# Optimization experiments

Hardware: AMD Instinct MI355X
Metric: run time of the kernel (lower is better)

The kernel has to match this reference:

```python
import jax, jax.numpy as jnp
import numpy as np

N = 50000
E = 800000
NHID = 128
NOUT = 64
NLAYER = 4
BN_EPS = 1e-5


def setup_inputs() -> dict:
    key = jax.random.key(0)
    ks = jax.random.split(key, 4)
    x = jax.random.normal(ks[0], (N, NHID), dtype=jnp.float32)
    edge_index = jax.random.randint(ks[1], (2, E), 0, N, dtype=jnp.int32)
    Ws = jax.random.normal(ks[2], (NLAYER, NHID, NHID), dtype=jnp.float32) / np.sqrt(NHID)
    bs = jnp.zeros((NLAYER, NHID), dtype=jnp.float32)
    gammas = jnp.ones((NLAYER, NHID), dtype=jnp.float32)
    betas = jnp.zeros((NLAYER, NHID), dtype=jnp.float32)
    Wout = jax.random.normal(ks[3], (NHID, NOUT), dtype=jnp.float32) / np.sqrt(NHID)
    bout = jnp.zeros((NOUT,), dtype=jnp.float32)
    return {"x": x, "edge_index": edge_index, "Ws": Ws, "bs": bs,
            "gammas": gammas, "betas": betas, "Wout": Wout, "bout": bout}


def _gcn_conv(x, src, dst, norm, W, b):
    # GCNConv: h = x W, then symmetric-normalized scatter-add over edges (+ self loops already in src/dst)
    h = x @ W                                   # [N, nhid]
    msgs = h[src] * norm[:, None]               # [E+N, nhid] gather + scale
    agg = jax.ops.segment_sum(msgs, dst, num_segments=N)  # scatter-add
    return agg + b


def _batchnorm(x, gamma, beta):
    mean = jnp.mean(x, axis=0)
    var = jnp.mean(jnp.square(x - mean), axis=0)  # biased var (torch BN)
    return (x - mean) * jax.lax.rsqrt(var + BN_EPS) * gamma + beta


def reference(x, edge_index, Ws, bs, gammas, betas, Wout, bout):
    # add self loops
    loops = jnp.arange(N, dtype=edge_index.dtype)
    src = jnp.concatenate([edge_index[0], loops])
    dst = jnp.concatenate([edge_index[1], loops])
    # symmetric degree normalization: deg^-1/2[src] * deg^-1/2[dst]
    deg = jax.ops.segment_sum(jnp.ones_like(dst, dtype=x.dtype), dst, num_segments=N)
    dinv = jax.lax.rsqrt(jnp.maximum(deg, 1.0))
    norm = dinv[src] * dinv[dst]

    prev = x
    for l in range(NLAYER):
        h = _gcn_conv(x, src, dst, norm, Ws[l], bs[l])
        h = _batchnorm(h, gammas[l], betas[l])
        h = jax.nn.relu(h)
        # dropout p=0.0 -> identity
        x = h + prev  # residual
        prev = x
    return x @ Wout + bout
```

## Files before the change

### kernel.cpp

```cpp
#include <hip/hip_runtime.h>

#define NN 50000
#define NE 800000
#define NH 128
#define NO 64
#define NL 4
#define BN_EPS 1e-5f
#define NB1 ((NN + 255) / 256)
#define NGB (NN / 16)

typedef __attribute__((ext_vector_type(8))) short short8;
typedef __attribute__((ext_vector_type(4))) float f32x4;

__device__ inline unsigned short f2bf(float f) {
    unsigned int u = __float_as_uint(f);
    return (unsigned short)((u + 0x7fffu + ((u >> 16) & 1u)) >> 16);
}
__device__ inline float bflo(unsigned int u) { return __uint_as_float(u << 16); }
__device__ inline float bfhi(unsigned int u) { return __uint_as_float(u & 0xffff0000u); }
__device__ inline unsigned pk(float a, float b) {
    return (unsigned)f2bf(a) | ((unsigned)f2bf(b) << 16);
}

__global__ void k_degrank(const int* __restrict__ dst, int* __restrict__ deg,
                          int* __restrict__ rank) {
    int base = (blockIdx.x * 256 + threadIdx.x) * 2;
    if (base >= NE) return;
    int2 d2 = *(const int2*)&dst[base];
    int2 r2;
    r2.x = atomicAdd(&deg[d2.x], 1);
    r2.y = atomicAdd(&deg[d2.y], 1);
    *(int2*)&rank[base] = r2;
}

__global__ void k_scan1(const int* __restrict__ deg, int* __restrict__ off,
                        int* __restrict__ aux, float* __restrict__ dinv) {
    __shared__ int ls[256];
    int i = blockIdx.x * 256 + threadIdx.x;
    int v = (i < NN) ? deg[i] : 0;
    ls[threadIdx.x] = v;
    __syncthreads();
    for (int s = 1; s < 256; s <<= 1) {
        int t = (threadIdx.x >= s) ? ls[threadIdx.x - s] : 0;
        __syncthreads();
        ls[threadIdx.x] += t;
        __syncthreads();
    }
    if (i < NN) {
        off[i] = ls[threadIdx.x] - v;
        dinv[i] = rsqrtf((float)v + 1.0f);
    }
    if (threadIdx.x == 255) aux[blockIdx.x] = ls[255];
}

__global__ void k_scan2(int* __restrict__ aux) {
    __shared__ int ls[256];
    int v = (threadIdx.x < NB1) ? aux[threadIdx.x] : 0;
    ls[threadIdx.x] = v;
    __syncthreads();
    for (int s = 1; s < 256; s <<= 1) {
        int t = (threadIdx.x >= s) ? ls[threadIdx.x - s] : 0;
        __syncthreads();
        ls[threadIdx.x] += t;
        __syncthreads();
    }
    if (threadIdx.x < NB1) aux[threadIdx.x] = ls[threadIdx.x] - v;
}

__global__ void k_fill(const int* __restrict__ src, const int* __restrict__ dst,
                       const int* __restrict__ off, const int* __restrict__ aux,
                       const int* __restrict__ rank, int* __restrict__ csr) {
    int base = (blockIdx.x * 256 + threadIdx.x) * 4;
    if (base >= NE) return;
    int4 d4 = *(const int4*)&dst[base];
    int4 r4 = *(const int4*)&rank[base];
    int4 s4 = *(const int4*)&src[base];
    csr[off[d4.x] + aux[d4.x >> 8] + r4.x] = s4.x;
    csr[off[d4.y] + aux[d4.y >> 8] + r4.y] = s4.y;
    csr[off[d4.z] + aux[d4.z >> 8] + r4.z] = s4.z;
    csr[off[d4.w] + aux[d4.w >> 8] + r4.w] = s4.w;
}

__global__ void k_pack(const float* __restrict__ Ws, const float* __restrict__ Wout,
                       unsigned short* __restrict__ Wpk, unsigned short* __restrict__ Wopk) {
    int t = blockIdx.x * 256 + threadIdx.x;
    if (t < NL * 16384) {
        int l = t >> 14, r = t & 16383;
        int ks = r >> 12, ct = (r >> 9) & 7, lane = (r >> 3) & 63, i = r & 7;
        int k = ks * 32 + (lane >> 4) * 8 + i;
        int n = ct * 16 + (lane & 15);
        Wpk[t] = f2bf(Ws[l * 16384 + k * 128 + n]);
    } else if (t < NL * 16384 + 8192) {
        int r = t - NL * 16384;
        int ks = r >> 11, ct = (r >> 9) & 3, lane = (r >> 3) & 63, i = r & 7;
        int k = ks * 32 + (lane >> 4) * 8 + i;
        int n = ct * 16 + (lane & 15);
        Wopk[r] = f2bf(Wout[k * 64 + n]);
    }
}

__global__ __launch_bounds__(256) void k_fg0(const float* __restrict__ X,
                                             const unsigned short* __restrict__ Wpk,
                                             const float* __restrict__ dinv,
                                             unsigned short* __restrict__ Hd) {
    int w = threadIdx.x >> 6, l = threadIdx.x & 63;
    int row0 = blockIdx.x * 64 + w * 16;
    int lo = l & 15, hi = l >> 4;
    int arow = row0 + lo;
    int crow = (arow < NN) ? arow : NN - 1;
    short8 frag[4];
#pragma unroll
    for (int g = 0; g < 4; g++) {
        int cs = g * 32 + hi * 8;
        float4 p0 = *(const float4*)&X[(size_t)crow * NH + cs];
        float4 p1 = *(const float4*)&X[(size_t)crow * NH + cs + 4];
        short8 f;
        f[0] = (short)f2bf(p0.x); f[1] = (short)f2bf(p0.y);
        f[2] = (short)f2bf(p0.z); f[3] = (short)f2bf(p0.w);
        f[4] = (short)f2bf(p1.x); f[5] = (short)f2bf(p1.y);
        f[6] = (short)f2bf(p1.z); f[7] = (short)f2bf(p1.w);
        frag[g] = f;
    }
    const short8* Wv = (const short8*)Wpk;
    int srow = row0 + hi * 4;
    float dv[4];
#pragma unroll
    for (int r = 0; r < 4; r++) dv[r] = (srow + r < NN) ? dinv[srow + r] : 0.0f;
#pragma unroll
    for (int ct = 0; ct < 8; ct++) {
        f32x4 acc = {0.0f, 0.0f, 0.0f, 0.0f};
#pragma unroll
        for (int g = 0; g < 4; g++)
            acc = __builtin_amdgcn_mfma_f32_16x16x32_bf16(frag[g], Wv[(g * 8 + ct) * 64 + l], acc, 0, 0, 0);
        int col = ct * 16 + lo;
#pragma unroll
        for (int r = 0; r < 4; r++) {
            int grow = srow + r;
            if (grow < NN) Hd[grow * NH + col] = f2bf(acc[r] * dv[r]);
        }
    }
}

__global__ __launch_bounds__(256) void k_fg(const unsigned short* __restrict__ AGGb,
                                            const float* __restrict__ scale,
                                            const float* __restrict__ shift,
                                            const float* __restrict__ Xprev,
                                            float* __restrict__ Xout,
                                            const unsigned short* __restrict__ Wpk,
                                            const float* __restrict__ dinv,
                                            unsigned short* __restrict__ Hd) {
    int w = threadIdx.x >> 6, l = threadIdx.x & 63;
    int row0 = blockIdx.x * 64 + w * 16;
    int lo = l & 15, hi = l >> 4;
    int arow = row0 + lo;
    bool valid = arow < NN;
    int crow = valid ? arow : NN - 1;
    short8 frag[4];
#pragma unroll
    for (int g = 0; g < 4; g++) {
        int cs = g * 32 + hi * 8;
        uint4 ab = *(const uint4*)&AGGb[(size_t)crow * NH + cs];
        float4 p0 = *(const float4*)&Xprev[(size_t)crow * NH + cs];
        float4 p1 = *(const float4*)&Xprev[(size_t)crow * NH + cs + 4];
        float4 sc0 = *(const float4*)&scale[cs];
        float4 sc1 = *(const float4*)&scale[cs + 4];
        float4 sh0 = *(const float4*)&shift[cs];
        float4 sh1 = *(const float4*)&shift[cs + 4];
        float o0 = fmaxf(fmaf(bflo(ab.x), sc0.x, sh0.x), 0.0f) + p0.x;
        float o1 = fmaxf(fmaf(bfhi(ab.x), sc0.y, sh0.y), 0.0f) + p0.y;
        float o2 = fmaxf(fmaf(bflo(ab.y), sc0.z, sh0.z), 0.0f) + p0.z;
        float o3 = fmaxf(fmaf(bfhi(ab.y), sc0.w, sh0.w), 0.0f) + p0.w;
        float o4 = fmaxf(fmaf(bflo(ab.z), sc1.x, sh1.x), 0.0f) + p1.x;
        float o5 = fmaxf(fmaf(bfhi(ab.z), sc1.y, sh1.y), 0.0f) + p1.y;
        float o6 = fmaxf(fmaf(bflo(ab.w), sc1.z, sh1.z), 0.0f) + p1.z;
        float o7 = fmaxf(fmaf(bfhi(ab.w), sc1.w, sh1.w), 0.0f) + p1.w;
        if (valid) {
            float4 s0 = {o0, o1, o2, o3}, s1 = {o4, o5, o6, o7};
            *(float4*)&Xout[(size_t)arow * NH + cs] = s0;
            *(float4*)&Xout[(size_t)arow * NH + cs + 4] = s1;
        }
        short8 f;
        f[0] = (short)f2bf(o0); f[1] = (short)f2bf(o1);
        f[2] = (short)f2bf(o2); f[3] = (short)f2bf(o3);
        f[4] = (short)f2bf(o4); f[5] = (short)f2bf(o5);
        f[6] = (short)f2bf(o6); f[7] = (short)f2bf(o7);
        frag[g] = f;
    }
    const short8* Wv = (const short8*)Wpk;
    int srow = row0 + hi * 4;
    float dv[4];
#pragma unroll
    for (int r = 0; r < 4; r++) dv[r] = (srow + r < NN) ? dinv[srow + r] : 0.0f;
#pragma unroll
    for (int ct = 0; ct < 8; ct++) {
        f32x4 acc = {0.0f, 0.0f, 0.0f, 0.0f};
#pragma unroll
        for (int g = 0; g < 4; g++)
            acc = __builtin_amdgcn_mfma_f32_16x16x32_bf16(frag[g], Wv[(g * 8 + ct) * 64 + l], acc, 0, 0, 0);
        int col = ct * 16 + lo;
#pragma unroll
        for (int r = 0; r < 4; r++) {
            int grow = srow + r;
            if (grow < NN) Hd[grow * NH + col] = f2bf(acc[r] * dv[r]);
        }
    }
}

__global__ __launch_bounds__(256) void k_fgout(const unsigned short* __restrict__ AGGb,
                                               const float* __restrict__ scale,
                                               const float* __restrict__ shift,
                                               const float* __restrict__ Xprev,
                                               const unsigned short* __restrict__ Wpk,
                                               const float* __restrict__ b,
                                               float* __restrict__ out) {
    int w = threadIdx.x >> 6, l = threadIdx.x & 63;
    int row0 = blockIdx.x * 64 + w * 16;
    int lo = l & 15, hi = l >> 4;
    int arow = row0 + lo;
    int crow = (arow < NN) ? arow : NN - 1;
    short8 frag[4];
#pragma unroll
    for (int g = 0; g < 4; g++) {
        int cs = g * 32 + hi * 8;
        uint4 ab = *(const uint4*)&AGGb[(size_t)crow * NH + cs];
        float4 p0 = *(const float4*)&Xprev[(size_t)crow * NH + cs];
        float4 p1 = *(const float4*)&Xprev[(size_t)crow * NH + cs + 4];
        float4 sc0 = *(const float4*)&scale[cs];
        float4 sc1 = *(const float4*)&scale[cs + 4];
        float4 sh0 = *(const float4*)&shift[cs];
        float4 sh1 = *(const float4*)&shift[cs + 4];
        short8 f;
        f[0] = (short)f2bf(fmaxf(fmaf(bflo(ab.x), sc0.x, sh0.x), 0.0f) + p0.x);
        f[1] = (short)f2bf(fmaxf(fmaf(bfhi(ab.x), sc0.y, sh0.y), 0.0f) + p0.y);
        f[2] = (short)f2bf(fmaxf(fmaf(bflo(ab.y), sc0.z, sh0.z), 0.0f) + p0.z);
        f[3] = (short)f2bf(fmaxf(fmaf(bfhi(ab.y), sc0.w, sh0.w), 0.0f) + p0.w);
        f[4] = (short)f2bf(fmaxf(fmaf(bflo(ab.z), sc1.x, sh1.x), 0.0f) + p1.x);
        f[5] = (short)f2bf(fmaxf(fmaf(bfhi(ab.z), sc1.y, sh1.y), 0.0f) + p1.y);
        f[6] = (short)f2bf(fmaxf(fmaf(bflo(ab.w), sc1.z, sh1.z), 0.0f) + p1.z);
        f[7] = (short)f2bf(fmaxf(fmaf(bfhi(ab.w), sc1.w, sh1.w), 0.0f) + p1.w);
        frag[g] = f;
    }
    const short8* Wv = (const short8*)Wpk;
    int srow = row0 + hi * 4;
#pragma unroll
    for (int ct = 0; ct < 4; ct++) {
        f32x4 acc = {0.0f, 0.0f, 0.0f, 0.0f};
#pragma unroll
        for (int g = 0; g < 4; g++)
            acc = __builtin_amdgcn_mfma_f32_16x16x32_bf16(frag[g], Wv[(g * 4 + ct) * 64 + l], acc, 0, 0, 0);
        int col = ct * 16 + lo;
        float bb = b[col];
#pragma unroll
        for (int r = 0; r < 4; r++) {
            int grow = srow + r;
            if (grow < NN) out[grow * NO + col] = acc[r] + bb;
        }
    }
}

__global__ __launch_bounds__(256) void k_gather(const unsigned short* __restrict__ Hd,
                                                const int* __restrict__ csr,
                                                const int* __restrict__ off,
                                                const int* __restrict__ aux,
                                                const int* __restrict__ deg,
                                                const float* __restrict__ dinv,
                                                unsigned short* __restrict__ AGGb,
                                                float* __restrict__ partial) {
    int b = blockIdx.x;
    int slot = threadIdx.x >> 4, q = threadIdx.x & 15;
    int g = b * 16 + slot;
    float a0 = 0, a1 = 0, a2 = 0, a3 = 0, a4 = 0, a5 = 0, a6 = 0, a7 = 0;
    if (g < NN) {
        const uint4* Hv = (const uint4*)Hd;
        int o = off[g] + aux[g >> 8];
        int d = deg[g];
        uint4 h = Hv[g * 16 + q];
        a0 = bflo(h.x); a1 = bfhi(h.x);
        a2 = bflo(h.y); a3 = bfhi(h.y);
        a4 = bflo(h.z); a5 = bfhi(h.z);
        a6 = bflo(h.w); a7 = bfhi(h.w);
        int j = 0;
        for (; j + 4 <= d; j += 4) {
            int s0 = csr[o + j], s1 = csr[o + j + 1];
            int s2 = csr[o + j + 2], s3 = csr[o + j + 3];
            uint4 h0 = Hv[s0 * 16 + q];
            uint4 h1 = Hv[s1 * 16 + q];
            uint4 h2 = Hv[s2 * 16 + q];
            uint4 h3 = Hv[s3 * 16 + q];
            a0 += (bflo(h0.x) + bflo(h1.x)) + (bflo(h2.x) + bflo(h3.x));
            a1 += (bfhi(h0.x) + bfhi(h1.x)) + (bfhi(h2.x) + bfhi(h3.x));
            a2 += (bflo(h0.y) + bflo(h1.y)) + (bflo(h2.y) + bflo(h3.y));
            a3 += (bfhi(h0.y) + bfhi(h1.y)) + (bfhi(h2.y) + bfhi(h3.y));
            a4 += (bflo(h0.z) + bflo(h1.z)) + (bflo(h2.z) + bflo(h3.z));
            a5 += (bfhi(h0.z) + bfhi(h1.z)) + (bfhi(h2.z) + bfhi(h3.z));
            a6 += (bflo(h0.w) + bflo(h1.w)) + (bflo(h2.w) + bflo(h3.w));
            a7 += (bfhi(h0.w) + bfhi(h1.w)) + (bfhi(h2.w) + bfhi(h3.w));
        }
        for (; j < d; j++) {
            int s0 = csr[o + j];
            uint4 h0 = Hv[s0 * 16 + q];
            a0 += bflo(h0.x); a1 += bfhi(h0.x);
            a2 += bflo(h0.y); a3 += bfhi(h0.y);
            a4 += bflo(h0.z); a5 += bfhi(h0.z);
            a6 += bflo(h0.w); a7 += bfhi(h0.w);
        }
        float dv = dinv[g];
        a0 *= dv; a1 *= dv; a2 *= dv; a3 *= dv;
        a4 *= dv; a5 *= dv; a6 *= dv; a7 *= dv;
        uint4 u;
        u.x = pk(a0, a1); u.y = pk(a2, a3);
        u.z = pk(a4, a5); u.w = pk(a6, a7);
        ((uint4*)AGGb)[g * 16 + q] = u;
    }
    float t0 = a0 * a0, t1 = a1 * a1, t2 = a2 * a2, t3 = a3 * a3;
    float t4 = a4 * a4, t5 = a5 * a5, t6 = a6 * a6, t7 = a7 * a7;
#define RED(v) v += __shfl_xor(v, 16); v += __shfl_xor(v, 32);
    RED(a0) RED(a1) RED(a2) RED(a3) RED(a4) RED(a5) RED(a6) RED(a7)
    RED(t0) RED(t1) RED(t2) RED(t3) RED(t4) RED(t5) RED(t6) RED(t7)
#undef RED
    __shared__ float ws[4][16][16];
    int wv = threadIdx.x >> 6, lane = threadIdx.x & 63;
    if (lane < 16) {
        ws[wv][lane][0] = a0; ws[wv][lane][1] = a1;
        ws[wv][lane][2] = a2; ws[wv][lane][3] = a3;
        ws[wv][lane][4] = a4; ws[wv][lane][5] = a5;
        ws[wv][lane][6] = a6; ws[wv][lane][7] = a7;
        ws[wv][lane][8] = t0; ws[wv][lane][9] = t1;
        ws[wv][lane][10] = t2; ws[wv][lane][11] = t3;
        ws[wv][lane][12] = t4; ws[wv][lane][13] = t5;
        ws[wv][lane][14] = t6; ws[wv][lane][15] = t7;
    }
    __syncthreads();
    if (threadIdx.x < 16) {
        int qq = threadIdx.x;
#pragma unroll
        for (int k = 0; k < 8; k++) {
            float sv = ws[0][qq][k] + ws[1][qq][k] + ws[2][qq][k] + ws[3][qq][k];
            float qv = ws[0][qq][k + 8] + ws[1][qq][k + 8] + ws[2][qq][k + 8] + ws[3][qq][k + 8];
            partial[(size_t)b * 256 + qq * 8 + k] = sv;
            partial[(size_t)b * 256 + 128 + qq * 8 + k] = qv;
        }
    }
}

__global__ __launch_bounds__(256) void k_statred(const float* __restrict__ partial,
                                                 const float* __restrict__ gamma,
                                                 const float* __restrict__ beta,
                                                 float* __restrict__ scale,
                                                 float* __restrict__ shift) {
    int s = blockIdx.x;
    int t = threadIdx.x;
    float sum = 0.0f, sq = 0.0f;
    for (int k = t; k < NGB; k += 256) {
        sum += partial[(size_t)k * 256 + s];
        sq  += partial[(size_t)k * 256 + 128 + s];
    }
    __shared__ float ls[256], lq[256];
    ls[t] = sum; lq[t] = sq;
    __syncthreads();
    for (int st = 128; st > 0; st >>= 1) {
        if (t < st) { ls[t] += ls[t + st]; lq[t] += lq[t + st]; }
        __syncthreads();
    }
    if (t == 0) {
        float mean = ls[0] * (1.0f / NN);
        float var = lq[0] * (1.0f / NN) - mean * mean;
        float istd = rsqrtf(var + BN_EPS);
        float sc = istd * gamma[s];
        scale[s] = sc;
        shift[s] = beta[s] - mean * sc;
    }
}

extern "C" void kernel_launch(void* const* d_in, const int* in_sizes, int n_in,
                              void* d_out, int out_size, void* d_ws, size_t ws_size,
                              hipStream_t stream) {
    const float* x    = (const float*)d_in[0];
    const int*   ei   = (const int*)d_in[1];
    const float* Ws   = (const float*)d_in[2];
    const float* gam  = (const float*)d_in[4];
    const float* bet  = (const float*)d_in[5];
    const float* Wout = (const float*)d_in[6];
    const float* bout = (const float*)d_in[7];
    float* out = (float*)d_out;

    const int* src = ei;
    const int* dst = ei + NE;

    char* p = (char*)d_ws;
    auto alloc = [&](size_t bytes) { char* r = p; p += (bytes + 255) & ~(size_t)255; return r; };
    int*   deg_i = (int*)alloc(NN * 4);
    int*   off   = (int*)alloc(NN * 4);
    int*   rank  = (int*)alloc((size_t)NE * 4);
    int*   aux   = (int*)alloc(256 * 4);
    int*   csr   = (int*)alloc((size_t)NE * 4);
    float* dinv  = (float*)alloc(NN * 4);
    float* XA    = (float*)alloc((size_t)NN * NH * 4);
    float* XB    = (float*)alloc((size_t)NN * NH * 4);
    unsigned short* Hd   = (unsigned short*)alloc((size_t)NN * NH * 2);
    unsigned short* AGGb = (unsigned short*)alloc((size_t)NN * NH * 2);
    unsigned short* Wpk  = (unsigned short*)alloc((size_t)NL * NH * NH * 2);
    unsigned short* Wopk = (unsigned short*)alloc((size_t)NH * NO * 2);
    float* partial = (float*)alloc((size_t)NGB * 256 * 4);
    float* scale = (float*)alloc(NH * 4);
    float* shift = (float*)alloc(NH * 4);

    hipMemsetAsync(deg_i, 0, NN * 4, stream);
    k_degrank<<<(NE / 2 + 255) / 256, 256, 0, stream>>>(dst, deg_i, rank);
    k_scan1<<<NB1, 256, 0, stream>>>(deg_i, off, aux, dinv);
    k_scan2<<<1, 256, 0, stream>>>(aux);
    k_fill<<<(NE / 4 + 255) / 256, 256, 0, stream>>>(src, dst, off, aux, rank, csr);
    k_pack<<<(NL * 16384 + 8192 + 255) / 256, 256, 0, stream>>>(Ws, Wout, Wpk, Wopk);

    const int GB = (NN + 63) / 64;

    k_fg0<<<GB, 256, 0, stream>>>(x, Wpk, dinv, Hd);

    const float* xprev = x;
    for (int l = 0; l < NL; l++) {
        k_gather<<<NGB, 256, 0, stream>>>(Hd, csr, off, aux, deg_i, dinv, AGGb, partial);
        k_statred<<<128, 256, 0, stream>>>(partial, gam + l * NH, bet + l * NH, scale, shift);
        if (l < NL - 1) {
            float* Xout = (l & 1) ? XB : XA;
            k_fg<<<GB, 256, 0, stream>>>(AGGb, scale, shift, xprev, Xout,
                                         Wpk + (size_t)(l + 1) * 16384, dinv, Hd);
            xprev = Xout;
        } else {
            k_fgout<<<GB, 256, 0, stream>>>(AGGb, scale, shift, xprev, Wopk, bout, out);
        }
    }
}
```

Measured before the change: 320.4 us.

## Store H and AGG in 32-column feature panels and gather per panel

H and AGG are stored as four column panels of 32 bf16 each, one per 32 features. The gather kernel now runs one block per (panel, 64-node chunk), with 4 lanes per node instead of 16. Each panel (about 3.2MB) can then stay cache-resident while it is gathered, improving locality of the random reads, at the cost of reading the CSR index list four times. The degree-count atomics are also split across four replicated counters to reduce contention, which needs per-replica offset arrays in the scan and fill. CSR loads use nontemporal hints, and the BN partial-stats layout and reduction are updated to match.

```diff
diff --git a/kernel.cpp b/kernel.cpp
--- a/kernel.cpp
+++ b/kernel.cpp
@@ -7,7 +7,8 @@
 #define NL 4
 #define BN_EPS 1e-5f
 #define NB1 ((NN + 255) / 256)
-#define NGB (NN / 16)
+#define NPB ((NN + 63) / 64)
+#define NPANEL 4
 
 typedef __attribute__((ext_vector_type(8))) short short8;
 typedef __attribute__((ext_vector_type(4))) float f32x4;
@@ -22,22 +23,30 @@
     return (unsigned)f2bf(a) | ((unsigned)f2bf(b) << 16);
 }
 
-__global__ void k_degrank(const int* __restrict__ dst, int* __restrict__ deg,
+__global__ void k_degrank(const int* __restrict__ dst, int* __restrict__ deg_r,
                           int* __restrict__ rank) {
     int base = (blockIdx.x * 256 + threadIdx.x) * 2;
     if (base >= NE) return;
     int2 d2 = *(const int2*)&dst[base];
-    int2 r2;
-    r2.x = atomicAdd(&deg[d2.x], 1);
-    r2.y = atomicAdd(&deg[d2.y], 1);
-    *(int2*)&rank[base] = r2;
-}
-
-__global__ void k_scan1(const int* __restrict__ deg, int* __restrict__ off,
-                        int* __restrict__ aux, float* __restrict__ dinv) {
+    int r0 = (base >> 9) & 3;
+    int r1 = ((base + 1) >> 9) & 3;
+    int2 rr;
+    rr.x = atomicAdd(&deg_r[r0 * NN + d2.x], 1);
+    rr.y = atomicAdd(&deg_r[r1 * NN + d2.y], 1);
+    *(int2*)&rank[base] = rr;
+}
+
+__global__ void k_scan1(const int* __restrict__ deg_r, int* __restrict__ off,
+                        int* __restrict__ aux, float* __restrict__ dinv,
+                        int* __restrict__ degT, int* __restrict__ offR) {
     __shared__ int ls[256];
     int i = blockIdx.x * 256 + threadIdx.x;
-    int v = (i < NN) ? deg[i] : 0;
+    int c0 = 0, c1 = 0, c2 = 0, c3 = 0;
+    if (i < NN) {
+        c0 = deg_r[i]; c1 = deg_r[NN + i];
+        c2 = deg_r[2 * NN + i]; c3 = deg_r[3 * NN + i];
+    }
+    int v = c0 + c1 + c2 + c3;
     ls[threadIdx.x] = v;
     __syncthreads();
     for (int s = 1; s < 256; s <<= 1) {
@@ -49,6 +58,11 @@
     if (i < NN) {
         off[i] = ls[threadIdx.x] - v;
         dinv[i] = rsqrtf((float)v + 1.0f);
+        degT[i] = v;
+        offR[i] = 0;
+        offR[NN + i] = c0;
+        offR[2 * NN + i] = c0 + c1;
+        offR[3 * NN + i] = c0 + c1 + c2;
     }
     if (threadIdx.x == 255) aux[blockIdx.x] = ls[255];
 }
@@ -69,16 +83,18 @@
 
 __global__ void k_fill(const int* __restrict__ src, const int* __restrict__ dst,
                        const int* __restrict__ off, const int* __restrict__ aux,
-                       const int* __restrict__ rank, int* __restrict__ csr) {
+                       const int* __restrict__ offR, const int* __restrict__ rank,
+                       int* __restrict__ csr) {
     int base = (blockIdx.x * 256 + threadIdx.x) * 4;
     if (base >= NE) return;
     int4 d4 = *(const int4*)&dst[base];
     int4 r4 = *(const int4*)&rank[base];
     int4 s4 = *(const int4*)&src[base];
-    csr[off[d4.x] + aux[d4.x >> 8] + r4.x] = s4.x;
-    csr[off[d4.y] + aux[d4.y >> 8] + r4.y] = s4.y;
-    csr[off[d4.z] + aux[d4.z >> 8] + r4.z] = s4.z;
-    csr[off[d4.w] + aux[d4.w >> 8] + r4.w] = s4.w;
+    const int* oR = offR + ((base >> 9) & 3) * NN;
+    csr[off[d4.x] + aux[d4.x >> 8] + oR[d4.x] + r4.x] = s4.x;
+    csr[off[d4.y] + aux[d4.y >> 8] + oR[d4.y] + r4.y] = s4.y;
+    csr[off[d4.z] + aux[d4.z >> 8] + oR[d4.z] + r4.z] = s4.z;
+    csr[off[d4.w] + aux[d4.w >> 8] + oR[d4.w] + r4.w] = s4.w;
 }
 
 __global__ void k_pack(const float* __restrict__ Ws, const float* __restrict__ Wout,
@@ -99,6 +115,7 @@
     }
 }
 
+
 __global__ __launch_bounds__(256) void k_fg0(const float* __restrict__ X,
                                              const unsigned short* __restrict__ Wpk,
                                              const float* __restrict__ dinv,
@@ -132,11 +149,11 @@
 #pragma unroll
         for (int g = 0; g < 4; g++)
             acc = __builtin_amdgcn_mfma_f32_16x16x32_bf16(frag[g], Wv[(g * 8 + ct) * 64 + l], acc, 0, 0, 0);
-        int col = ct * 16 + lo;
+        int panel = ct >> 1, within = (ct & 1) * 16 + lo;
 #pragma unroll
         for (int r = 0; r < 4; r++) {
             int grow = srow + r;
-            if (grow < NN) Hd[grow * NH + col] = f2bf(acc[r] * dv[r]);
+            if (grow < NN) Hd[((size_t)panel * NN + grow) * 32 + within] = f2bf(acc[r] * dv[r]);
         }
     }
 }
@@ -159,7 +176,7 @@
 #pragma unroll
     for (int g = 0; g < 4; g++) {
         int cs = g * 32 + hi * 8;
-        uint4 ab = *(const uint4*)&AGGb[(size_t)crow * NH + cs];
+        uint4 ab = ((const uint4*)AGGb)[((size_t)g * NN + crow) * 4 + hi];
         float4 p0 = *(const float4*)&Xprev[(size_t)crow * NH + cs];
         float4 p1 = *(const float4*)&Xprev[(size_t)crow * NH + cs + 4];
         float4 sc0 = *(const float4*)&scale[cs];
@@ -197,11 +214,11 @@
 #pragma unroll
         for (int g = 0; g < 4; g++)
             acc = __builtin_amdgcn_mfma_f32_16x16x32_bf16(frag[g], Wv[(g * 8 + ct) * 64 + l], acc, 0, 0, 0);
-        int col = ct * 16 + lo;
+        int panel = ct >> 1, within = (ct & 1) * 16 + lo;
 #pragma unroll
         for (int r = 0; r < 4; r++) {
             int grow = srow + r;
-            if (grow < NN) Hd[grow * NH + col] = f2bf(acc[r] * dv[r]);
+            if (grow < NN) Hd[((size_t)panel * NN + grow) * 32 + within] = f2bf(acc[r] * dv[r]);
         }
     }
 }
@@ -222,7 +239,7 @@
 #pragma unroll
     for (int g = 0; g < 4; g++) {
         int cs = g * 32 + hi * 8;
-        uint4 ab = *(const uint4*)&AGGb[(size_t)crow * NH + cs];
+        uint4 ab = ((const uint4*)AGGb)[((size_t)g * NN + crow) * 4 + hi];
         float4 p0 = *(const float4*)&Xprev[(size_t)crow * NH + cs];
         float4 p1 = *(const float4*)&Xprev[(size_t)crow * NH + cs + 4];
         float4 sc0 = *(const float4*)&scale[cs];
@@ -262,31 +279,35 @@
                                                 const int* __restrict__ csr,
                                                 const int* __restrict__ off,
                                                 const int* __restrict__ aux,
-                                                const int* __restrict__ deg,
+                                                const int* __restrict__ degT,
                                                 const float* __restrict__ dinv,
                                                 unsigned short* __restrict__ AGGb,
                                                 float* __restrict__ partial) {
-    int b = blockIdx.x;
-    int slot = threadIdx.x >> 4, q = threadIdx.x & 15;
-    int g = b * 16 + slot;
+    int bid = blockIdx.x;
+    int panel = bid / NPB, nb = bid - panel * NPB;
+    int slot = threadIdx.x >> 2, q = threadIdx.x & 3;
+    int g = nb * 64 + slot;
     float a0 = 0, a1 = 0, a2 = 0, a3 = 0, a4 = 0, a5 = 0, a6 = 0, a7 = 0;
     if (g < NN) {
         const uint4* Hv = (const uint4*)Hd;
+        size_t pb = (size_t)panel * NN;
         int o = off[g] + aux[g >> 8];
-        int d = deg[g];
-        uint4 h = Hv[g * 16 + q];
+        int d = degT[g];
+        uint4 h = Hv[(pb + g) * 4 + q];
         a0 = bflo(h.x); a1 = bfhi(h.x);
         a2 = bflo(h.y); a3 = bfhi(h.y);
         a4 = bflo(h.z); a5 = bfhi(h.z);
         a6 = bflo(h.w); a7 = bfhi(h.w);
         int j = 0;
         for (; j + 4 <= d; j += 4) {
-            int s0 = csr[o + j], s1 = csr[o + j + 1];
-            int s2 = csr[o + j + 2], s3 = csr[o + j + 3];
-            uint4 h0 = Hv[s0 * 16 + q];
-            uint4 h1 = Hv[s1 * 16 + q];
-            uint4 h2 = Hv[s2 * 16 + q];
-            uint4 h3 = Hv[s3 * 16 + q];
+            int s0 = __builtin_nontemporal_load(&csr[o + j]);
+            int s1 = __builtin_nontemporal_load(&csr[o + j + 1]);
+            int s2 = __builtin_nontemporal_load(&csr[o + j + 2]);
+            int s3 = __builtin_nontemporal_load(&csr[o + j + 3]);
+            uint4 h0 = Hv[(pb + s0) * 4 + q];
+            uint4 h1 = Hv[(pb + s1) * 4 + q];
+            uint4 h2 = Hv[(pb + s2) * 4 + q];
+            uint4 h3 = Hv[(pb + s3) * 4 + q];
             a0 += (bflo(h0.x) + bflo(h1.x)) + (bflo(h2.x) + bflo(h3.x));
             a1 += (bfhi(h0.x) + bfhi(h1.x)) + (bfhi(h2.x) + bfhi(h3.x));
             a2 += (bflo(h0.y) + bflo(h1.y)) + (bflo(h2.y) + bflo(h3.y));
@@ -297,8 +318,8 @@
             a7 += (bfhi(h0.w) + bfhi(h1.w)) + (bfhi(h2.w) + bfhi(h3.w));
         }
         for (; j < d; j++) {
-            int s0 = csr[o + j];
-            uint4 h0 = Hv[s0 * 16 + q];
+            int s0 = __builtin_nontemporal_load(&csr[o + j]);
+            uint4 h0 = Hv[(pb + s0) * 4 + q];
             a0 += bflo(h0.x); a1 += bfhi(h0.x);
             a2 += bflo(h0.y); a3 += bfhi(h0.y);
             a4 += bflo(h0.z); a5 += bfhi(h0.z);
@@ -310,36 +331,33 @@
         uint4 u;
         u.x = pk(a0, a1); u.y = pk(a2, a3);
         u.z = pk(a4, a5); u.w = pk(a6, a7);
-        ((uint4*)AGGb)[g * 16 + q] = u;
+        ((uint4*)AGGb)[(pb + g) * 4 + q] = u;
     }
     float t0 = a0 * a0, t1 = a1 * a1, t2 = a2 * a2, t3 = a3 * a3;
     float t4 = a4 * a4, t5 = a5 * a5, t6 = a6 * a6, t7 = a7 * a7;
-#define RED(v) v += __shfl_xor(v, 16); v += __shfl_xor(v, 32);
+#define RED(v) v += __shfl_xor(v, 4); v += __shfl_xor(v, 8); v += __shfl_xor(v, 16); v += __shfl_xor(v, 32);
     RED(a0) RED(a1) RED(a2) RED(a3) RED(a4) RED(a5) RED(a6) RED(a7)
     RED(t0) RED(t1) RED(t2) RED(t3) RED(t4) RED(t5) RED(t6) RED(t7)
 #undef RED
-    __shared__ float ws[4][16][16];
+    __shared__ float wsS[4][4][8], wsQ[4][4][8];
     int wv = threadIdx.x >> 6, lane = threadIdx.x & 63;
-    if (lane < 16) {
-        ws[wv][lane][0] = a0; ws[wv][lane][1] = a1;
-        ws[wv][lane][2] = a2; ws[wv][lane][3] = a3;
-        ws[wv][lane][4] = a4; ws[wv][lane][5] = a5;
-        ws[wv][lane][6] = a6; ws[wv][lane][7] = a7;
-        ws[wv][lane][8] = t0; ws[wv][lane][9] = t1;
-        ws[wv][lane][10] = t2; ws[wv][lane][11] = t3;
-        ws[wv][lane][12] = t4; ws[wv][lane][13] = t5;
-        ws[wv][lane][14] = t6; ws[wv][lane][15] = t7;
+    if (lane < 4) {
+        wsS[wv][lane][0] = a0; wsS[wv][lane][1] = a1;
+        wsS[wv][lane][2] = a2; wsS[wv][lane][3] = a3;
+        wsS[wv][lane][4] = a4; wsS[wv][lane][5] = a5;
+        wsS[wv][lane][6] = a6; wsS[wv][lane][7] = a7;
+        wsQ[wv][lane][0] = t0; wsQ[wv][lane][1] = t1;
+        wsQ[wv][lane][2] = t2; wsQ[wv][lane][3] = t3;
+        wsQ[wv][lane][4] = t4; wsQ[wv][lane][5] = t5;
+        wsQ[wv][lane][6] = t6; wsQ[wv][lane][7] = t7;
     }
     __syncthreads();
-    if (threadIdx.x < 16) {
-        int qq = threadIdx.x;
-#pragma unroll
-        for (int k = 0; k < 8; k++) {
-            float sv = ws[0][qq][k] + ws[1][qq][k] + ws[2][qq][k] + ws[3][qq][k];
-            float qv = ws[0][qq][k + 8] + ws[1][qq][k + 8] + ws[2][qq][k + 8] + ws[3][qq][k + 8];
-            partial[(size_t)b * 256 + qq * 8 + k] = sv;
-            partial[(size_t)b * 256 + 128 + qq * 8 + k] = qv;
-        }
+    if (threadIdx.x < 32) {
+        int qq = threadIdx.x >> 3, k = threadIdx.x & 7;
+        float s = wsS[0][qq][k] + wsS[1][qq][k] + wsS[2][qq][k] + wsS[3][qq][k];
+        float s2 = wsQ[0][qq][k] + wsQ[1][qq][k] + wsQ[2][qq][k] + wsQ[3][qq][k];
+        partial[(size_t)bid * 64 + qq * 8 + k] = s;
+        partial[(size_t)bid * 64 + 32 + qq * 8 + k] = s2;
     }
 }
 
@@ -348,12 +366,14 @@
                                                  const float* __restrict__ beta,
                                                  float* __restrict__ scale,
                                                  float* __restrict__ shift) {
-    int s = blockIdx.x;
+    int c = blockIdx.x;
+    int panel = c >> 5, wv = c & 31;
     int t = threadIdx.x;
     float sum = 0.0f, sq = 0.0f;
-    for (int k = t; k < NGB; k += 256) {
-        sum += partial[(size_t)k * 256 + s];
-        sq  += partial[(size_t)k * 256 + 128 + s];
+    for (int nb = t; nb < NPB; nb += 256) {
+        size_t base = ((size_t)(panel * NPB + nb)) * 64;
+        sum += partial[base + wv];
+        sq  += partial[base + 32 + wv];
     }
     __shared__ float ls[256], lq[256];
     ls[t] = sum; lq[t] = sq;
@@ -366,9 +386,9 @@
         float mean = ls[0] * (1.0f / NN);
         float var = lq[0] * (1.0f / NN) - mean * mean;
         float istd = rsqrtf(var + BN_EPS);
-        float sc = istd * gamma[s];
-        scale[s] = sc;
-        shift[s] = beta[s] - mean * sc;
+        float sc = istd * gamma[c];
+        scale[c] = sc;
+        shift[c] = beta[c] - mean * sc;
     }
 }
 
@@ -389,7 +409,9 @@
 
     char* p = (char*)d_ws;
     auto alloc = [&](size_t bytes) { char* r = p; p += (bytes + 255) & ~(size_t)255; return r; };
-    int*   deg_i = (int*)alloc(NN * 4);
+    int*   deg_r = (int*)alloc((size_t)4 * NN * 4);
+    int*   offR  = (int*)alloc((size_t)4 * NN * 4);
+    int*   degT  = (int*)alloc(NN * 4);
     int*   off   = (int*)alloc(NN * 4);
     int*   rank  = (int*)alloc((size_t)NE * 4);
     int*   aux   = (int*)alloc(256 * 4);
@@ -401,15 +423,15 @@
     unsigned short* AGGb = (unsigned short*)alloc((size_t)NN * NH * 2);
     unsigned short* Wpk  = (unsigned short*)alloc((size_t)NL * NH * NH * 2);
     unsigned short* Wopk = (unsigned short*)alloc((size_t)NH * NO * 2);
-    float* partial = (float*)alloc((size_t)NGB * 256 * 4);
+    float* partial = (float*)alloc((size_t)NPANEL * NPB * 64 * 4);
     float* scale = (float*)alloc(NH * 4);
     float* shift = (float*)alloc(NH * 4);
 
-    hipMemsetAsync(deg_i, 0, NN * 4, stream);
-    k_degrank<<<(NE / 2 + 255) / 256, 256, 0, stream>>>(dst, deg_i, rank);
-    k_scan1<<<NB1, 256, 0, stream>>>(deg_i, off, aux, dinv);
+    hipMemsetAsync(deg_r, 0, (size_t)4 * NN * 4, stream);
+    k_degrank<<<(NE / 2 + 255) / 256, 256, 0, stream>>>(dst, deg_r, rank);
+    k_scan1<<<NB1, 256, 0, stream>>>(deg_r, off, aux, dinv, degT, offR);
     k_scan2<<<1, 256, 0, stream>>>(aux);
-    k_fill<<<(NE / 4 + 255) / 256, 256, 0, stream>>>(src, dst, off, aux, rank, csr);
+    k_fill<<<(NE / 4 + 255) / 256, 256, 0, stream>>>(src, dst, off, aux, offR, rank, csr);
     k_pack<<<(NL * 16384 + 8192 + 255) / 256, 256, 0, stream>>>(Ws, Wout, Wpk, Wopk);
 
     const int GB = (NN + 63) / 64;
@@ -418,7 +440,7 @@
 
     const float* xprev = x;
     for (int l = 0; l < NL; l++) {
-        k_gather<<<NGB, 256, 0, stream>>>(Hd, csr, off, aux, deg_i, dinv, AGGb, partial);
+        k_gather<<<NPANEL * NPB, 256, 0, stream>>>(Hd, csr, off, aux, degT, dinv, AGGb, partial);
         k_statred<<<128, 256, 0, stream>>>(partial, gam + l * NH, bet + l * NH, scale, shift);
         if (l < NL - 1) {
             float* Xout = (l & 1) ? XB : XA;
```

Measured after the change: 357.1 us. 1.11x slower.

## Split neighbor gather across two half-groups per node and shard degree atomics

Applied to the files above, without the earlier changes.

The gather kernel now assigns 32 threads (two 16-lane halves) per node, each half summing half of the neighbor list, and combines them with a lane shuffle. This doubles parallelism and memory-level concurrency for the latency-bound gather. CSR construction shards the degree atomic counters into four replicas keyed by edge chunk to reduce atomic contention, with per-replica offsets added during fill. Nontemporal loads and stores are used for CSR indices and outputs. This adds extra offset arrays, a larger memset, and more partial-stat blocks for the statistics reduction.

```diff
diff --git a/kernel.cpp b/kernel.cpp
--- a/kernel.cpp
+++ b/kernel.cpp
@@ -7,10 +7,11 @@
 #define NL 4
 #define BN_EPS 1e-5f
 #define NB1 ((NN + 255) / 256)
-#define NGB (NN / 16)
+#define NGB (NN / 8)
 
 typedef __attribute__((ext_vector_type(8))) short short8;
 typedef __attribute__((ext_vector_type(4))) float f32x4;
+typedef __attribute__((ext_vector_type(4))) unsigned int u32x4;
 
 __device__ inline unsigned short f2bf(float f) {
     unsigned int u = __float_as_uint(f);
@@ -22,22 +23,29 @@
     return (unsigned)f2bf(a) | ((unsigned)f2bf(b) << 16);
 }
 
-__global__ void k_degrank(const int* __restrict__ dst, int* __restrict__ deg,
+__global__ void k_degrank(const int* __restrict__ dst, int* __restrict__ deg_r,
                           int* __restrict__ rank) {
     int base = (blockIdx.x * 256 + threadIdx.x) * 2;
     if (base >= NE) return;
     int2 d2 = *(const int2*)&dst[base];
-    int2 r2;
-    r2.x = atomicAdd(&deg[d2.x], 1);
-    r2.y = atomicAdd(&deg[d2.y], 1);
-    *(int2*)&rank[base] = r2;
-}
-
-__global__ void k_scan1(const int* __restrict__ deg, int* __restrict__ off,
-                        int* __restrict__ aux, float* __restrict__ dinv) {
+    int r0 = (base >> 9) & 3;
+    int2 rr;
+    rr.x = atomicAdd(&deg_r[r0 * NN + d2.x], 1);
+    rr.y = atomicAdd(&deg_r[r0 * NN + d2.y], 1);
+    *(int2*)&rank[base] = rr;
+}
+
+__global__ void k_scan1(const int* __restrict__ deg_r, int* __restrict__ off,
+                        int* __restrict__ aux, float* __restrict__ dinv,
+                        int* __restrict__ degT, int* __restrict__ offR) {
     __shared__ int ls[256];
     int i = blockIdx.x * 256 + threadIdx.x;
-    int v = (i < NN) ? deg[i] : 0;
+    int c0 = 0, c1 = 0, c2 = 0, c3 = 0;
+    if (i < NN) {
+        c0 = deg_r[i]; c1 = deg_r[NN + i];
+        c2 = deg_r[2 * NN + i]; c3 = deg_r[3 * NN + i];
+    }
+    int v = c0 + c1 + c2 + c3;
     ls[threadIdx.x] = v;
     __syncthreads();
     for (int s = 1; s < 256; s <<= 1) {
@@ -49,6 +57,11 @@
     if (i < NN) {
         off[i] = ls[threadIdx.x] - v;
         dinv[i] = rsqrtf((float)v + 1.0f);
+        degT[i] = v;
+        offR[i] = 0;
+        offR[NN + i] = c0;
+        offR[2 * NN + i] = c0 + c1;
+        offR[3 * NN + i] = c0 + c1 + c2;
     }
     if (threadIdx.x == 255) aux[blockIdx.x] = ls[255];
 }
@@ -69,16 +82,18 @@
 
 __global__ void k_fill(const int* __restrict__ src, const int* __restrict__ dst,
                        const int* __restrict__ off, const int* __restrict__ aux,
-                       const int* __restrict__ rank, int* __restrict__ csr) {
+                       const int* __restrict__ offR, const int* __restrict__ rank,
+                       int* __restrict__ csr) {
     int base = (blockIdx.x * 256 + threadIdx.x) * 4;
     if (base >= NE) return;
     int4 d4 = *(const int4*)&dst[base];
     int4 r4 = *(const int4*)&rank[base];
     int4 s4 = *(const int4*)&src[base];
-    csr[off[d4.x] + aux[d4.x >> 8] + r4.x] = s4.x;
-    csr[off[d4.y] + aux[d4.y >> 8] + r4.y] = s4.y;
-    csr[off[d4.z] + aux[d4.z >> 8] + r4.z] = s4.z;
-    csr[off[d4.w] + aux[d4.w >> 8] + r4.w] = s4.w;
+    const int* oR = offR + ((base >> 9) & 3) * NN;
+    csr[off[d4.x] + aux[d4.x >> 8] + oR[d4.x] + r4.x] = s4.x;
+    csr[off[d4.y] + aux[d4.y >> 8] + oR[d4.y] + r4.y] = s4.y;
+    csr[off[d4.z] + aux[d4.z >> 8] + oR[d4.z] + r4.z] = s4.z;
+    csr[off[d4.w] + aux[d4.w >> 8] + oR[d4.w] + r4.w] = s4.w;
 }
 
 __global__ void k_pack(const float* __restrict__ Ws, const float* __restrict__ Wout,
@@ -262,59 +277,71 @@
                                                 const int* __restrict__ csr,
                                                 const int* __restrict__ off,
                                                 const int* __restrict__ aux,
-                                                const int* __restrict__ deg,
+                                                const int* __restrict__ degT,
                                                 const float* __restrict__ dinv,
                                                 unsigned short* __restrict__ AGGb,
                                                 float* __restrict__ partial) {
     int b = blockIdx.x;
-    int slot = threadIdx.x >> 4, q = threadIdx.x & 15;
-    int g = b * 16 + slot;
+    int slot = threadIdx.x >> 5;
+    int half = (threadIdx.x >> 4) & 1;
+    int q = threadIdx.x & 15;
+    int g = b * 8 + slot;
+    const u32x4* Hv = (const u32x4*)Hd;
+    int o = off[g] + aux[g >> 8];
+    int d = degT[g];
     float a0 = 0, a1 = 0, a2 = 0, a3 = 0, a4 = 0, a5 = 0, a6 = 0, a7 = 0;
-    if (g < NN) {
-        const uint4* Hv = (const uint4*)Hd;
-        int o = off[g] + aux[g >> 8];
-        int d = deg[g];
-        uint4 h = Hv[g * 16 + q];
+    if (!half) {
+        u32x4 h = Hv[g * 16 + q];
         a0 = bflo(h.x); a1 = bfhi(h.x);
         a2 = bflo(h.y); a3 = bfhi(h.y);
         a4 = bflo(h.z); a5 = bfhi(h.z);
         a6 = bflo(h.w); a7 = bfhi(h.w);
-        int j = 0;
-        for (; j + 4 <= d; j += 4) {
-            int s0 = csr[o + j], s1 = csr[o + j + 1];
-            int s2 = csr[o + j + 2], s3 = csr[o + j + 3];
-            uint4 h0 = Hv[s0 * 16 + q];
-            uint4 h1 = Hv[s1 * 16 + q];
-            uint4 h2 = Hv[s2 * 16 + q];
-            uint4 h3 = Hv[s3 * 16 + q];
-            a0 += (bflo(h0.x) + bflo(h1.x)) + (bflo(h2.x) + bflo(h3.x));
-            a1 += (bfhi(h0.x) + bfhi(h1.x)) + (bfhi(h2.x) + bfhi(h3.x));
-            a2 += (bflo(h0.y) + bflo(h1.y)) + (bflo(h2.y) + bflo(h3.y));
-            a3 += (bfhi(h0.y) + bfhi(h1.y)) + (bfhi(h2.y) + bfhi(h3.y));
-            a4 += (bflo(h0.z) + bflo(h1.z)) + (bflo(h2.z) + bflo(h3.z));
-            a5 += (bfhi(h0.z) + bfhi(h1.z)) + (bfhi(h2.z) + bfhi(h3.z));
-            a6 += (bflo(h0.w) + bflo(h1.w)) + (bflo(h2.w) + bflo(h3.w));
-            a7 += (bfhi(h0.w) + bfhi(h1.w)) + (bfhi(h2.w) + bfhi(h3.w));
-        }
-        for (; j < d; j++) {
-            int s0 = csr[o + j];
-            uint4 h0 = Hv[s0 * 16 + q];
-            a0 += bflo(h0.x); a1 += bfhi(h0.x);
-            a2 += bflo(h0.y); a3 += bfhi(h0.y);
-            a4 += bflo(h0.z); a5 += bfhi(h0.z);
-            a6 += bflo(h0.w); a7 += bfhi(h0.w);
-        }
-        float dv = dinv[g];
-        a0 *= dv; a1 *= dv; a2 *= dv; a3 *= dv;
-        a4 *= dv; a5 *= dv; a6 *= dv; a7 *= dv;
-        uint4 u;
+    }
+    int dh = d >> 1;
+    int j = half ? dh : 0;
+    int je = half ? d : dh;
+    for (; j + 4 <= je; j += 4) {
+        int s0 = __builtin_nontemporal_load(&csr[o + j]);
+        int s1 = __builtin_nontemporal_load(&csr[o + j + 1]);
+        int s2 = __builtin_nontemporal_load(&csr[o + j + 2]);
+        int s3 = __builtin_nontemporal_load(&csr[o + j + 3]);
+        u32x4 h0 = Hv[s0 * 16 + q];
+        u32x4 h1 = Hv[s1 * 16 + q];
+        u32x4 h2 = Hv[s2 * 16 + q];
+        u32x4 h3 = Hv[s3 * 16 + q];
+        a0 += (bflo(h0.x) + bflo(h1.x)) + (bflo(h2.x) + bflo(h3.x));
+        a1 += (bfhi(h0.x) + bfhi(h1.x)) + (bfhi(h2.x) + bfhi(h3.x));
+        a2 += (bflo(h0.y) + bflo(h1.y)) + (bflo(h2.y) + bflo(h3.y));
+        a3 += (bfhi(h0.y) + bfhi(h1.y)) + (bfhi(h2.y) + bfhi(h3.y));
+        a4 += (bflo(h0.z) + bflo(h1.z)) + (bflo(h2.z) + bflo(h3.z));
+        a5 += (bfhi(h0.z) + bfhi(h1.z)) + (bfhi(h2.z) + bfhi(h3.z));
+        a6 += (bflo(h0.w) + bflo(h1.w)) + (bflo(h2.w) + bflo(h3.w));
+        a7 += (bfhi(h0.w) + bfhi(h1.w)) + (bfhi(h2.w) + bfhi(h3.w));
+    }
+    for (; j < je; j++) {
+        int s0 = __builtin_nontemporal_load(&csr[o + j]);
+        u32x4 h0 = Hv[s0 * 16 + q];
+        a0 += bflo(h0.x); a1 += bfhi(h0.x);
+        a2 += bflo(h0.y); a3 += bfhi(h0.y);
+        a4 += bflo(h0.z); a5 += bfhi(h0.z);
+        a6 += bflo(h0.w); a7 += bfhi(h0.w);
+    }
+    a0 += __shfl_xor(a0, 16); a1 += __shfl_xor(a1, 16);
+    a2 += __shfl_xor(a2, 16); a3 += __shfl_xor(a3, 16);
+    a4 += __shfl_xor(a4, 16); a5 += __shfl_xor(a5, 16);
+    a6 += __shfl_xor(a6, 16); a7 += __shfl_xor(a7, 16);
+    float dv = dinv[g];
+    a0 *= dv; a1 *= dv; a2 *= dv; a3 *= dv;
+    a4 *= dv; a5 *= dv; a6 *= dv; a7 *= dv;
+    if (!half) {
+        u32x4 u;
         u.x = pk(a0, a1); u.y = pk(a2, a3);
         u.z = pk(a4, a5); u.w = pk(a6, a7);
-        ((uint4*)AGGb)[g * 16 + q] = u;
+        __builtin_nontemporal_store(u, &((u32x4*)AGGb)[g * 16 + q]);
     }
     float t0 = a0 * a0, t1 = a1 * a1, t2 = a2 * a2, t3 = a3 * a3;
     float t4 = a4 * a4, t5 = a5 * a5, t6 = a6 * a6, t7 = a7 * a7;
-#define RED(v) v += __shfl_xor(v, 16); v += __shfl_xor(v, 32);
+#define RED(v) v += __shfl_xor(v, 32);
     RED(a0) RED(a1) RED(a2) RED(a3) RED(a4) RED(a5) RED(a6) RED(a7)
     RED(t0) RED(t1) RED(t2) RED(t3) RED(t4) RED(t5) RED(t6) RED(t7)
 #undef RED
@@ -337,8 +364,8 @@
         for (int k = 0; k < 8; k++) {
             float sv = ws[0][qq][k] + ws[1][qq][k] + ws[2][qq][k] + ws[3][qq][k];
             float qv = ws[0][qq][k + 8] + ws[1][qq][k + 8] + ws[2][qq][k + 8] + ws[3][qq][k + 8];
-            partial[(size_t)b * 256 + qq * 8 + k] = sv;
-            partial[(size_t)b * 256 + 128 + qq * 8 + k] = qv;
+            __builtin_nontemporal_store(sv, &partial[(size_t)b * 256 + qq * 8 + k]);
+            __builtin_nontemporal_store(qv, &partial[(size_t)b * 256 + 128 + qq * 8 + k]);
         }
     }
 }
@@ -389,7 +416,9 @@
 
     char* p = (char*)d_ws;
     auto alloc = [&](size_t bytes) { char* r = p; p += (bytes + 255) & ~(size_t)255; return r; };
-    int*   deg_i = (int*)alloc(NN * 4);
+    int*   deg_r = (int*)alloc((size_t)4 * NN * 4);
+    int*   offR  = (int*)alloc((size_t)4 * NN * 4);
+    int*   degT  = (int*)alloc(NN * 4);
     int*   off   = (int*)alloc(NN * 4);
     int*   rank  = (int*)alloc((size_t)NE * 4);
     int*   aux   = (int*)alloc(256 * 4);
@@ -405,11 +434,11 @@
     float* scale = (float*)alloc(NH * 4);
     float* shift = (float*)alloc(NH * 4);
 
-    hipMemsetAsync(deg_i, 0, NN * 4, stream);
-    k_degrank<<<(NE / 2 + 255) / 256, 256, 0, stream>>>(dst, deg_i, rank);
-    k_scan1<<<NB1, 256, 0, stream>>>(deg_i, off, aux, dinv);
+    hipMemsetAsync(deg_r, 0, (size_t)4 * NN * 4, stream);
+    k_degrank<<<(NE / 2 + 255) / 256, 256, 0, stream>>>(dst, deg_r, rank);
+    k_scan1<<<NB1, 256, 0, stream>>>(deg_r, off, aux, dinv, degT, offR);
     k_scan2<<<1, 256, 0, stream>>>(aux);
-    k_fill<<<(NE / 4 + 255) / 256, 256, 0, stream>>>(src, dst, off, aux, rank, csr);
+    k_fill<<<(NE / 4 + 255) / 256, 256, 0, stream>>>(src, dst, off, aux, offR, rank, csr);
     k_pack<<<(NL * 16384 + 8192 + 255) / 256, 256, 0, stream>>>(Ws, Wout, Wpk, Wopk);
 
     const int GB = (NN + 63) / 64;
@@ -418,7 +447,7 @@
 
     const float* xprev = x;
     for (int l = 0; l < NL; l++) {
-        k_gather<<<NGB, 256, 0, stream>>>(Hd, csr, off, aux, deg_i, dinv, AGGb, partial);
+        k_gather<<<NGB, 256, 0, stream>>>(Hd, csr, off, aux, degT, dinv, AGGb, partial);
         k_statred<<<128, 256, 0, stream>>>(partial, gam + l * NH, bet + l * NH, scale, shift);
         if (l < NL - 1) {
             float* Xout = (l & 1) ? XB : XA;
```

New measurement: 396.1 us. +23.6%, slower.
